# Kernel tuning notes

Measured on AMD Instinct MI355X. Metric: run time of the kernel, lower is better.

The kernel has to match this reference:

```python
import jax, jax.numpy as jnp
import numpy as np

EMB_SIZE = 100000
EMB_DIM = 256
HALF = EMB_DIM // 2
B = 65536
K = 5


def setup_inputs() -> dict:
    key = jax.random.key(0)
    ks = jax.random.split(key, 9)
    initrange = 1.0 / EMB_DIM
    u_l = jax.random.uniform(ks[0], (EMB_SIZE, HALF), jnp.float32, -initrange, initrange)
    u_r = jax.random.uniform(ks[1], (EMB_SIZE, HALF), jnp.float32, -initrange, initrange)
    # torch init is zeros for v tables; use small random so grads/outputs are nontrivial
    v_l = jax.random.uniform(ks[2], (EMB_SIZE, HALF), jnp.float32, -initrange, initrange)
    v_r = jax.random.uniform(ks[3], (EMB_SIZE, HALF), jnp.float32, -initrange, initrange)
    pos_u = jax.random.randint(ks[4], (B,), 0, EMB_SIZE)
    pos_v_l = jax.random.randint(ks[5], (B,), 0, EMB_SIZE)
    pos_v_r = jax.random.randint(ks[6], (B,), 0, EMB_SIZE)
    neg_v_l = jax.random.randint(ks[7], (B, K), 0, EMB_SIZE)
    neg_v_r = jax.random.randint(ks[8], (B, K), 0, EMB_SIZE)
    return {
        "u_l_weight": u_l, "u_r_weight": u_r,
        "v_l_weight": v_l, "v_r_weight": v_r,
        "pos_u": pos_u, "pos_v_l": pos_v_l, "pos_v_r": pos_v_r,
        "neg_v_l": neg_v_l, "neg_v_r": neg_v_r,
    }


def _neg_logsig(x):
    # -logsigmoid(x), numerically stable
    return -jax.nn.log_sigmoid(x)


def reference(u_l_weight, u_r_weight, v_l_weight, v_r_weight,
              pos_u, pos_v_l, pos_v_r, neg_v_l, neg_v_r):
    emb_u_l = u_l_weight[pos_u]          # [B, H]
    emb_u_r = u_r_weight[pos_u]          # [B, H]
    emb_v_l = v_l_weight[pos_v_l]        # [B, H]
    emb_v_r = v_r_weight[pos_v_r]        # [B, H]
    emb_neg_v_l = v_l_weight[neg_v_l]    # [B, K, H]
    emb_neg_v_r = v_r_weight[neg_v_r]    # [B, K, H]

    score_l = jnp.clip(jnp.sum(emb_u_l * emb_v_l, axis=1), -10.0, 10.0)
    score_l = _neg_logsig(score_l)
    score_r = jnp.clip(jnp.sum(emb_u_r * emb_v_r, axis=1), -10.0, 10.0)
    score_r = _neg_logsig(score_r)

    neg_score_l = jnp.clip(jnp.einsum('bkh,bh->bk', emb_neg_v_l, emb_u_l), -10.0, 10.0)
    neg_score_l = -jnp.sum(jax.nn.log_sigmoid(-neg_score_l), axis=1)
    neg_score_r = jnp.clip(jnp.einsum('bkh,bh->bk', emb_neg_v_r, emb_u_r), -10.0, 10.0)
    neg_score_r = -jnp.sum(jax.nn.log_sigmoid(-neg_score_r), axis=1)

    return jnp.mean(score_l + score_r + neg_score_l + neg_score_r)
```

## Files before the change

kernel.cpp:

```cpp
#include <hip/hip_runtime.h>


#define HV4   32
#define BATCH 65536
#define K     5

__device__ __forceinline__ float dot4(float4 a, float4 b) {
    return a.x * b.x + a.y * b.y + a.z * b.z + a.w * b.w;
}

__device__ __forceinline__ float red16(float v) {
    v += __shfl_xor(v, 8, 16);
    v += __shfl_xor(v, 4, 16);
    v += __shfl_xor(v, 2, 16);
    v += __shfl_xor(v, 1, 16);
    return v;
}

__device__ __forceinline__ float clip10(float x) {
    return fminf(fmaxf(x, -10.0f), 10.0f);
}

__global__ __launch_bounds__(256) void skipgram_fwd(
    const float* __restrict__ u_l, const float* __restrict__ u_r,
    const float* __restrict__ v_l, const float* __restrict__ v_r,
    const int* __restrict__ pos_u, const int* __restrict__ pos_vl,
    const int* __restrict__ pos_vr, const int* __restrict__ neg_vl,
    const int* __restrict__ neg_vr, float* __restrict__ out)
{
    const int tid  = threadIdx.x;
    const int lane = tid & 15;
    const int grp  = tid >> 4;
    const int b    = (blockIdx.x << 4) + grp;

    const int iu  = pos_u[b];
    const int ivl = pos_vl[b];
    const int ivr = pos_vr[b];

    const float4* ULr = (const float4*)u_l + (size_t)iu * HV4;
    const float4* URr = (const float4*)u_r + (size_t)iu * HV4;
    float4 ul0 = ULr[lane], ul1 = ULr[lane + 16];
    float4 ur0 = URr[lane], ur1 = URr[lane + 16];

    const float4* VLr = (const float4*)v_l + (size_t)ivl * HV4;
    const float4* VRr = (const float4*)v_r + (size_t)ivr * HV4;
    float4 vl0 = VLr[lane], vl1 = VLr[lane + 16];
    float4 vr0 = VRr[lane], vr1 = VRr[lane + 16];

    float sl = red16(dot4(ul0, vl0) + dot4(ul1, vl1));
    float sr = red16(dot4(ur0, vr0) + dot4(ur1, vr1));

    float acc = __logf(1.0f + __expf(-clip10(sl)))
              + __logf(1.0f + __expf(-clip10(sr)));

    #pragma unroll
    for (int k = 0; k < K; ++k) {
        const int inl = neg_vl[b * K + k];
        const int inr = neg_vr[b * K + k];
        const float4* NL = (const float4*)v_l + (size_t)inl * HV4;
        const float4* NR = (const float4*)v_r + (size_t)inr * HV4;
        float4 nl0 = NL[lane], nl1 = NL[lane + 16];
        float4 nr0 = NR[lane], nr1 = NR[lane + 16];
        float snl = red16(dot4(ul0, nl0) + dot4(ul1, nl1));
        float snr = red16(dot4(ur0, nr0) + dot4(ur1, nr1));
        acc += __logf(1.0f + __expf(clip10(snl)))
             + __logf(1.0f + __expf(clip10(snr)));
    }

    __shared__ float smem[16];
    if (lane == 0) smem[grp] = acc;
    __syncthreads();
    if (tid == 0) {
        float s = 0.0f;
        #pragma unroll
        for (int i = 0; i < 16; ++i) s += smem[i];
        atomicAdd(out, s * (1.0f / BATCH));
    }
}

extern "C" void kernel_launch(void* const* d_in, const int* in_sizes, int n_in,
                              void* d_out, int out_size, void* d_ws, size_t ws_size,
                              hipStream_t stream) {
    const float* u_l   = (const float*)d_in[0];
    const float* u_r   = (const float*)d_in[1];
    const float* v_l   = (const float*)d_in[2];
    const float* v_r   = (const float*)d_in[3];
    const int* pos_u   = (const int*)d_in[4];
    const int* pos_vl  = (const int*)d_in[5];
    const int* pos_vr  = (const int*)d_in[6];
    const int* neg_vl  = (const int*)d_in[7];
    const int* neg_vr  = (const int*)d_in[8];
    float* out = (float*)d_out;

    hipMemsetAsync(out, 0, sizeof(float), stream);

    skipgram_fwd<<<BATCH / 16, 256, 0, stream>>>(
        u_l, u_r, v_l, v_r, pos_u, pos_vl, pos_vr, neg_vl, neg_vr, out);
}
```

Before: 233.2 us.

## Issue all row gathers up front with 32 lanes per row and DPP reductions

Each batch element now uses 32 lanes, one float4 per lane per row, instead of 16 lanes holding two float4 each. All 14 embedding-row loads are issued back-to-back through inline asm before a single vmcnt wait, so the gathers stay in flight together. Shuffle reductions are replaced with DPP row operations, and the grid doubles to cover the batch. The cost is more registers held live and a reliance on the DPP row_bcast semantics being correct on this hardware.

New measurement: 270.5 us. 16.0% more time.

```diff
diff --git a/kernel.cpp b/kernel.cpp
--- a/kernel.cpp
+++ b/kernel.cpp
@@ -1,25 +1,37 @@
 #include <hip/hip_runtime.h>
 
 
-#define HV4   32
 #define BATCH 65536
 #define K     5
+
+__device__ __forceinline__ float clip10(float x) {
+    return fminf(fmaxf(x, -10.0f), 10.0f);
+}
 
 __device__ __forceinline__ float dot4(float4 a, float4 b) {
     return a.x * b.x + a.y * b.y + a.z * b.z + a.w * b.w;
 }
 
-__device__ __forceinline__ float red16(float v) {
-    v += __shfl_xor(v, 8, 16);
-    v += __shfl_xor(v, 4, 16);
-    v += __shfl_xor(v, 2, 16);
-    v += __shfl_xor(v, 1, 16);
-    return v;
+template<int CTRL, int RMASK = 0xf>
+__device__ __forceinline__ float dpp_add(float x) {
+    int y = __builtin_amdgcn_update_dpp(0, __float_as_int(x), CTRL, RMASK, 0xf, true);
+    return x + __int_as_float(y);
 }
 
-__device__ __forceinline__ float clip10(float x) {
-    return fminf(fmaxf(x, -10.0f), 10.0f);
+__device__ __forceinline__ float wsum32(float x) {
+    x = dpp_add<0x111>(x);
+    x = dpp_add<0x112>(x);
+    x = dpp_add<0x114>(x);
+    x = dpp_add<0x118>(x);
+    x = dpp_add<0x142, 0xa>(x);
+    return x;
 }
+
+#define LOAD_ROW(dst, base, idx)                                              \
+    {                                                                         \
+        const float4* _p = (const float4*)(base) + (((size_t)(idx)) << 5) + lig; \
+        asm volatile("global_load_dwordx4 %0, %1, off" : "=v"(dst) : "v"(_p)); \
+    }
 
 __global__ __launch_bounds__(256) void skipgram_fwd(
     const float* __restrict__ u_l, const float* __restrict__ u_r,
@@ -28,52 +40,71 @@
     const int* __restrict__ pos_vr, const int* __restrict__ neg_vl,
     const int* __restrict__ neg_vr, float* __restrict__ out)
 {
-    const int tid  = threadIdx.x;
-    const int lane = tid & 15;
-    const int grp  = tid >> 4;
-    const int b    = (blockIdx.x << 4) + grp;
+    const int tid = threadIdx.x;
+    const int lig = tid & 31;
+    const int e   = tid >> 5;
+    const int b   = (blockIdx.x << 3) + e;
 
     const int iu  = pos_u[b];
     const int ivl = pos_vl[b];
     const int ivr = pos_vr[b];
+    const int in0 = neg_vl[b * K + 0], in1 = neg_vl[b * K + 1],
+              in2 = neg_vl[b * K + 2], in3 = neg_vl[b * K + 3],
+              in4 = neg_vl[b * K + 4];
+    const int ir0 = neg_vr[b * K + 0], ir1 = neg_vr[b * K + 1],
+              ir2 = neg_vr[b * K + 2], ir3 = neg_vr[b * K + 3],
+              ir4 = neg_vr[b * K + 4];
 
-    const float4* ULr = (const float4*)u_l + (size_t)iu * HV4;
-    const float4* URr = (const float4*)u_r + (size_t)iu * HV4;
-    float4 ul0 = ULr[lane], ul1 = ULr[lane + 16];
-    float4 ur0 = URr[lane], ur1 = URr[lane + 16];
+    float4 rul, rur, rvl, rvr;
+    float4 nl0, nl1, nl2, nl3, nl4;
+    float4 nr0, nr1, nr2, nr3, nr4;
+    LOAD_ROW(rul, u_l, iu);
+    LOAD_ROW(rur, u_r, iu);
+    LOAD_ROW(rvl, v_l, ivl);
+    LOAD_ROW(rvr, v_r, ivr);
+    LOAD_ROW(nl0, v_l, in0);
+    LOAD_ROW(nl1, v_l, in1);
+    LOAD_ROW(nl2, v_l, in2);
+    LOAD_ROW(nl3, v_l, in3);
+    LOAD_ROW(nl4, v_l, in4);
+    LOAD_ROW(nr0, v_r, ir0);
+    LOAD_ROW(nr1, v_r, ir1);
+    LOAD_ROW(nr2, v_r, ir2);
+    LOAD_ROW(nr3, v_r, ir3);
+    LOAD_ROW(nr4, v_r, ir4);
 
-    const float4* VLr = (const float4*)v_l + (size_t)ivl * HV4;
-    const float4* VRr = (const float4*)v_r + (size_t)ivr * HV4;
-    float4 vl0 = VLr[lane], vl1 = VLr[lane + 16];
-    float4 vr0 = VRr[lane], vr1 = VRr[lane + 16];
+    asm volatile("s_waitcnt vmcnt(0)" ::: "memory");
+    __builtin_amdgcn_sched_barrier(0);
 
-    float sl = red16(dot4(ul0, vl0) + dot4(ul1, vl1));
-    float sr = red16(dot4(ur0, vr0) + dot4(ur1, vr1));
+    float p[12];
+    p[0]  = dot4(rul, rvl);
+    p[1]  = dot4(rur, rvr);
+    p[2]  = dot4(rul, nl0);
+    p[3]  = dot4(rul, nl1);
+    p[4]  = dot4(rul, nl2);
+    p[5]  = dot4(rul, nl3);
+    p[6]  = dot4(rul, nl4);
+    p[7]  = dot4(rur, nr0);
+    p[8]  = dot4(rur, nr1);
+    p[9]  = dot4(rur, nr2);
+    p[10] = dot4(rur, nr3);
+    p[11] = dot4(rur, nr4);
 
-    float acc = __logf(1.0f + __expf(-clip10(sl)))
-              + __logf(1.0f + __expf(-clip10(sr)));
-
+    float acc = 0.0f;
     #pragma unroll
-    for (int k = 0; k < K; ++k) {
-        const int inl = neg_vl[b * K + k];
-        const int inr = neg_vr[b * K + k];
-        const float4* NL = (const float4*)v_l + (size_t)inl * HV4;
-        const float4* NR = (const float4*)v_r + (size_t)inr * HV4;
-        float4 nl0 = NL[lane], nl1 = NL[lane + 16];
-        float4 nr0 = NR[lane], nr1 = NR[lane + 16];
-        float snl = red16(dot4(ul0, nl0) + dot4(ul1, nl1));
-        float snr = red16(dot4(ur0, nr0) + dot4(ur1, nr1));
-        acc += __logf(1.0f + __expf(clip10(snl)))
-             + __logf(1.0f + __expf(clip10(snr)));
+    for (int i = 0; i < 12; ++i) {
+        float s = clip10(wsum32(p[i]));
+        float x = (i < 2) ? -s : s;
+        acc += __logf(1.0f + __expf(x));
     }
 
-    __shared__ float smem[16];
-    if (lane == 0) smem[grp] = acc;
+    __shared__ float smem[8];
+    if (lig == 31) smem[e] = acc;
     __syncthreads();
     if (tid == 0) {
         float s = 0.0f;
         #pragma unroll
-        for (int i = 0; i < 16; ++i) s += smem[i];
+        for (int i = 0; i < 8; ++i) s += smem[i];
         atomicAdd(out, s * (1.0f / BATCH));
     }
 }
@@ -94,6 +125,6 @@
 
     hipMemsetAsync(out, 0, sizeof(float), stream);
 
-    skipgram_fwd<<<BATCH / 16, 256, 0, stream>>>(
+    skipgram_fwd<<<BATCH / 8, 256, 0, stream>>>(
         u_l, u_r, v_l, v_r, pos_u, pos_vl, pos_vr, neg_vl, neg_vr, out);
 }
```
